# Optimization experiments

Hardware: AMD Instinct MI355X
Metric: run time of the kernel (lower is better)

The kernel has to match this reference:

```python
import jax, jax.numpy as jnp
import numpy as np

N = 50000          # nodes per node type
E = 1_600_000      # edges per canonical etype (avg degree 32)
IN_F = 385         # BERT_EMBEDDING_DIM(384) + NUMERICAL_FEATURES(1)
H = 128            # HIDDEN_DIM
# ntype order: 0=Policy, 1=Control, 2=ComplianceRequirement, 3=Risk
# etypes (src_ntype, dst_ntype): implements, mitigates, violates, addresses, informs
ETYPES = [(0, 1), (1, 3), (3, 2), (0, 2), (2, 0)]


def setup_inputs() -> dict:
    key = jax.random.key(0)
    ks = jax.random.split(key, 12)
    inp = {}
    names = ["feat_policy", "feat_control", "feat_compliance", "feat_risk"]
    for i, n in enumerate(names):
        inp[n] = jax.random.normal(ks[i], (N, IN_F), jnp.float32)
    inp["src"] = jax.random.randint(ks[4], (5, E), 0, N, jnp.int32)
    inp["dst"] = jax.random.randint(ks[5], (5, E), 0, N, jnp.int32)
    s_in = 1.0 / np.sqrt(IN_F).astype(np.float32)
    s_h = np.sqrt(6.0 / (H + H)).astype(np.float32)  # xavier_uniform for GraphConv
    inp["Wp"] = jax.random.uniform(ks[6], (4, IN_F, H), jnp.float32, -s_in, s_in)
    inp["bp"] = jax.random.uniform(ks[7], (4, H), jnp.float32, -s_in, s_in)
    inp["Wc1"] = jax.random.uniform(ks[8], (5, H, H), jnp.float32, -s_h, s_h)
    inp["bc1"] = jnp.zeros((5, H), jnp.float32)
    inp["Wc2"] = jax.random.uniform(ks[9], (5, H, H), jnp.float32, -s_h, s_h)
    inp["bc2"] = jnp.zeros((5, H), jnp.float32)
    return inp


def _graph_conv(x, s, d, W, b):
    """DGL GraphConv(norm='both'): D_dst^{-1/2} A D_src^{-1/2} X W + b."""
    ones = jnp.ones(s.shape[0], x.dtype)
    deg_out = jnp.clip(jax.ops.segment_sum(ones, s, num_segments=N), 1.0)
    deg_in = jnp.clip(jax.ops.segment_sum(ones, d, num_segments=N), 1.0)
    xs = x * jax.lax.rsqrt(deg_out)[:, None]            # [N, H] scale by src out-deg
    agg = jax.ops.segment_sum(xs[s], d, num_segments=N)  # gather + scatter-sum [N, H]
    agg = agg * jax.lax.rsqrt(deg_in)[:, None]
    return agg @ W + b


def reference(feat_policy, feat_control, feat_compliance, feat_risk,
              src, dst, Wp, bp, Wc1, bc1, Wc2, bc2):
    feats = [feat_policy, feat_control, feat_compliance, feat_risk]
    # input projections + relu per node type
    h = [jax.nn.relu(f @ Wp[i] + bp[i]) for i, f in enumerate(feats)]

    def hetero_layer(h, Wc, bc):
        out = [jnp.zeros((N, H), h[0].dtype) for _ in range(4)]
        for k, (st, dt) in enumerate(ETYPES):  # HeteroGraphConv aggregate='sum'
            out[dt] = out[dt] + _graph_conv(h[st], src[k], dst[k], Wc[k], bc[k])
        return out

    h = [jax.nn.relu(v) for v in hetero_layer(h, Wc1, bc1)]
    h = [jax.nn.relu(v) for v in hetero_layer(h, Wc2, bc2)]
    return jnp.stack(h)  # [4, N, H] final embeddings per node type
```

## Files before the change

### kernel.cpp

```cpp
#include <hip/hip_runtime.h>
#include <hip/hip_bf16.h>

#define INF 385
#define HD 128
#define NWG 16
#define HIST_BLOCKS (10 * NWG)

typedef __attribute__((ext_vector_type(8))) short short8;
typedef __attribute__((ext_vector_type(4))) float f32x4;

__device__ inline unsigned short f2b(float f) {
    __hip_bfloat16 h = __float2bfloat16(f);
    return *reinterpret_cast<unsigned short*>(&h);
}
__device__ inline float b2f(unsigned int lo16) {
    union { unsigned int u; float f; } c; c.u = lo16 << 16; return c.f;
}

__device__ __forceinline__ void convert_body(
    const float* f0, const float* f1, const float* f2, const float* f3,
    unsigned int* featB, float* alast, int N, int gid, int nthr)
{
    int per = N * 192;
    int tot = 4 * per;
    for (int p = gid; p < tot; p += nthr) {
        int t = p / per, rem = p - t * per;
        int n = rem / 192, c2 = (rem - n * 192) * 2;
        const float* f = (t < 2) ? (t == 0 ? f0 : f1) : (t == 2 ? f2 : f3);
        const float* row = f + (size_t)n * INF;
        float a = row[c2], b = row[c2 + 1];
        featB[p] = ((unsigned int)f2b(b) << 16) | f2b(a);
    }
    for (int p = gid; p < 4 * N; p += nthr) {
        int t = p / N, n = p - t * N;
        const float* f = (t < 2) ? (t == 0 ? f0 : f1) : (t == 2 ? f2 : f3);
        alast[p] = f[(size_t)n * INF + 384];
    }
}

__global__ __launch_bounds__(1024) void hist_conv_kernel(
    const int* __restrict__ src_all, const int* __restrict__ dst_all,
    unsigned short* __restrict__ partial,
    unsigned short* __restrict__ rank_local,
    int E, int N,
    const float* __restrict__ f0, const float* __restrict__ f1,
    const float* __restrict__ f2, const float* __restrict__ f3,
    unsigned int* __restrict__ featB, float* __restrict__ alast)
{
    __shared__ unsigned int cnt[25000];
    int tid = threadIdx.x;
    if (blockIdx.x >= HIST_BLOCKS) {
        int nconv = gridDim.x - HIST_BLOCKS;
        convert_body(f0, f1, f2, f3, featB, alast, N,
                     (blockIdx.x - HIST_BLOCKS) * 1024 + tid, nconv * 1024);
        return;
    }
    int g = blockIdx.x / NWG;
    int w = blockIdx.x % NWG;
    int half = (N + 1) / 2;
    for (int i = tid; i < half; i += 1024) cnt[i] = 0;
    __syncthreads();

    int C = (E + NWG - 1) / NWG;
    int lo = w * C, hi = min(lo + C, E);
    if (g < 5) {
        const int* arr = dst_all + (size_t)g * E;
        for (int e = lo + tid; e < hi; e += 1024) {
            int d = __builtin_nontemporal_load(&arr[e]);
            unsigned int sh = (d & 1) * 16;
            unsigned int old = atomicAdd(&cnt[d >> 1], 1u << sh);
            rank_local[(size_t)g * E + e] = (unsigned short)((old >> sh) & 0xffffu);
        }
    } else {
        const int* arr = src_all + (size_t)(g - 5) * E;
        for (int e = lo + tid; e < hi; e += 1024) {
            int d = __builtin_nontemporal_load(&arr[e]);
            atomicAdd(&cnt[d >> 1], 1u << ((d & 1) * 16));
        }
    }
    __syncthreads();
    unsigned short* outp = partial + ((size_t)g * NWG + w) * N;
    for (int n = tid; n < N; n += 1024)
        outp[n] = (unsigned short)((cnt[n >> 1] >> ((n & 1) * 16)) & 0xffffu);
}

__global__ void reduce_kernel(unsigned short* __restrict__ partial, int* __restrict__ cnt_dst,
                              float* __restrict__ rsq_out, float* __restrict__ rsq_in, int N) {
    int i = blockIdx.x * blockDim.x + threadIdx.x;
    int stride = gridDim.x * blockDim.x;
    int tot = 10 * N;
    for (; i < tot; i += stride) {
        int g = i / N, n = i - g * N;
        unsigned short* p = partial + ((size_t)g * NWG) * N + n;
        int sum = 0;
        #pragma unroll
        for (int w = 0; w < NWG; ++w) {
            int v = p[(size_t)w * N];
            p[(size_t)w * N] = (unsigned short)sum;
            sum += v;
        }
        float r = rsqrtf((float)max(sum, 1));
        if (g < 5) { cnt_dst[i] = sum; rsq_in[i] = r; }
        else rsq_out[i - 5 * N] = r;
    }
}

__global__ __launch_bounds__(1024) void scan_kernel(const int* __restrict__ cnt_all,
                                                    int* __restrict__ off_all, int n) {
    const int* cnt = cnt_all + (size_t)blockIdx.x * n;
    int* off = off_all + (size_t)blockIdx.x * (n + 1);
    __shared__ int ssum[1024];
    int t = threadIdx.x;
    int chunk = (n + 1023) / 1024;
    int lo = t * chunk, hi = min(lo + chunk, n);
    int s = 0;
    for (int i = lo; i < hi; ++i) s += cnt[i];
    ssum[t] = s;
    __syncthreads();
    for (int d = 1; d < 1024; d <<= 1) {
        int v = (t >= d) ? ssum[t - d] : 0;
        __syncthreads();
        ssum[t] += v;
        __syncthreads();
    }
    int excl = (t == 0) ? 0 : ssum[t - 1];
    for (int i = lo; i < hi; ++i) { off[i] = excl; excl += cnt[i]; }
    if (t == 1023) off[n] = ssum[1023];
}

__global__ __launch_bounds__(256) void permute_kernel(
    const int* __restrict__ src_all, const int* __restrict__ dst_all,
    const int* __restrict__ off, const unsigned short* __restrict__ partial,
    const unsigned short* __restrict__ rank_local,
    unsigned short* __restrict__ sorted, int E, int N)
{
    int gid = blockIdx.x * blockDim.x + threadIdx.x;
    int nthr = gridDim.x * blockDim.x;
    int tot = 5 * E;
    int C = (E + NWG - 1) / NWG;
    for (int i0 = gid * 4; i0 < tot; i0 += nthr * 4) {
        int d[4], s[4], rl[4];
        #pragma unroll
        for (int j = 0; j < 4; ++j) {
            d[j]  = __builtin_nontemporal_load(&dst_all[i0 + j]);
            s[j]  = __builtin_nontemporal_load(&src_all[i0 + j]);
            rl[j] = __builtin_nontemporal_load(&rank_local[i0 + j]);
        }
        int pos[4];
        #pragma unroll
        for (int j = 0; j < 4; ++j) {
            int i = i0 + j;
            int k = i / E, e = i - k * E;
            int w = e / C;
            pos[j] = off[(size_t)k * (N + 1) + d[j]]
                   + partial[((size_t)k * NWG + w) * N + d[j]]
                   + rl[j] + k * E;
        }
        #pragma unroll
        for (int j = 0; j < 4; ++j)
            __builtin_nontemporal_store((unsigned short)s[j], &sorted[pos[j]]);
    }
}

__global__ void convert_kernel(const float* __restrict__ f0, const float* __restrict__ f1,
                               const float* __restrict__ f2, const float* __restrict__ f3,
                               unsigned int* __restrict__ featB, float* __restrict__ alast, int N) {
    convert_body(f0, f1, f2, f3, featB, alast, N,
                 blockIdx.x * blockDim.x + threadIdx.x, gridDim.x * blockDim.x);
}

__global__ void prep_weights_kernel(const float* __restrict__ Wp,
                                    const float* __restrict__ Wc1, const float* __restrict__ Wc2,
                                    const float* __restrict__ bc1, const float* __restrict__ bc2,
                                    unsigned short* __restrict__ WpT,
                                    unsigned short* __restrict__ WcT,
                                    float* __restrict__ cbias) {
    int i = blockIdx.x * blockDim.x + threadIdx.x;
    int stride = gridDim.x * blockDim.x;
    const int nWp = 4 * 128 * 384;
    for (int p = i; p < nWp; p += stride) {
        int t = p / (128 * 384), rem = p % (128 * 384);
        int c = rem / 384, k = rem % 384;
        WpT[p] = f2b(Wp[(size_t)t * INF * HD + (size_t)k * HD + c]);
    }
    const int nWc = 5 * 128 * 128;
    for (int p = i; p < 2 * nWc; p += stride) {
        int layer = p / nWc, rem = p % nWc;
        int e = rem / (128 * 128), rem2 = rem % (128 * 128);
        int c = rem2 / 128, k = rem2 % 128;
        const float* W = layer ? Wc2 : Wc1;
        WcT[p] = f2b(W[(size_t)e * 128 * 128 + (size_t)k * 128 + c]);
    }
    for (int p = i; p < 2 * 4 * 128; p += stride) {
        int layer = p / 512, rem = p % 512;
        int t = rem / 128, c = rem % 128;
        const float* bc = layer ? bc2 : bc1;
        float v;
        if (t == 0) v = bc[4 * 128 + c];
        else if (t == 1) v = bc[0 * 128 + c];
        else if (t == 2) v = bc[2 * 128 + c] + bc[3 * 128 + c];
        else v = bc[1 * 128 + c];
        cbias[p] = v;
    }
}

struct GemmDesc {
    const unsigned short* A;
    const unsigned short* Bt;
    const float* bias;
    const float* rowscale;
    const float* alast;
    const float* wlast;
    unsigned short* out;
};
struct GemmBatch { GemmDesc d[5]; };

__global__ __launch_bounds__(256) void gemm_mfma_kernel(
    GemmBatch batch, int lda, int M, int K, int relu)
{
    const GemmDesc dsc = batch.d[blockIdx.y];
    const unsigned short* __restrict__ Bt = dsc.Bt;
    const unsigned short* __restrict__ A = dsc.A;

    __shared__ __align__(16) unsigned short As[64][72];
    __shared__ __align__(16) unsigned short Bs[128][72];
    const int tid = threadIdx.x;
    const int bm = blockIdx.x * 64;
    const int wid = tid >> 6, lane = tid & 63;
    const int wr = wid & 1, wc = wid >> 1;
    const int l15 = lane & 15, l4 = lane >> 4;

    f32x4 acc[2][4] = {};

    for (int k0 = 0; k0 < K; k0 += 64) {
        {
            int r = tid >> 2, q = tid & 3;
            int gm = bm + r;
            if (gm < M) {
                const uint4* g = (const uint4*)(A + (size_t)gm * lda + k0 + q * 16);
                *(uint4*)&As[r][q * 16] = g[0];
                *(uint4*)&As[r][q * 16 + 8] = g[1];
            } else {
                uint4 z = {0, 0, 0, 0};
                *(uint4*)&As[r][q * 16] = z;
                *(uint4*)&As[r][q * 16 + 8] = z;
            }
        }
        {
            int col = tid >> 1, hf = tid & 1;
            const uint4* g = (const uint4*)(Bt + (size_t)col * K + k0 + hf * 32);
            #pragma unroll
            for (int j = 0; j < 4; ++j)
                *(uint4*)&Bs[col][hf * 32 + j * 8] = g[j];
        }
        __syncthreads();
        #pragma unroll
        for (int kk = 0; kk < 2; ++kk) {
            short8 a[2], b[4];
            #pragma unroll
            for (int mi = 0; mi < 2; ++mi)
                a[mi] = *(const short8*)&As[wr * 32 + mi * 16 + l15][kk * 32 + l4 * 8];
            #pragma unroll
            for (int ni = 0; ni < 4; ++ni)
                b[ni] = *(const short8*)&Bs[wc * 64 + ni * 16 + l15][kk * 32 + l4 * 8];
            #pragma unroll
            for (int mi = 0; mi < 2; ++mi)
                #pragma unroll
                for (int ni = 0; ni < 4; ++ni)
                    acc[mi][ni] = __builtin_amdgcn_mfma_f32_16x16x32_bf16(
                        a[mi], b[ni], acc[mi][ni], 0, 0, 0);
        }
        __syncthreads();
    }

    #pragma unroll
    for (int mi = 0; mi < 2; ++mi) {
        #pragma unroll
        for (int r = 0; r < 4; ++r) {
            int grow = bm + wr * 32 + mi * 16 + l4 * 4 + r;
            if (grow >= M) continue;
            float rs = dsc.rowscale ? dsc.rowscale[grow] : 1.f;
            float al = dsc.alast ? dsc.alast[grow] : 0.f;
            #pragma unroll
            for (int ni = 0; ni < 4; ++ni) {
                int gcol = wc * 64 + ni * 16 + l15;
                float v = acc[mi][ni][r];
                if (dsc.wlast) v += al * dsc.wlast[gcol];
                if (dsc.bias) v += dsc.bias[gcol];
                v *= rs;
                if (relu) v = fmaxf(v, 0.f);
                dsc.out[(size_t)grow * HD + gcol] = f2b(v);
            }
        }
    }
}

struct GatherDesc {
    const unsigned short* msgA; const unsigned short* sortedA;
    const int* offA; const float* rsqA;
    const unsigned short* msgB; const unsigned short* sortedB;
    const int* offB; const float* rsqB;
    const float* bias; void* out;
};
struct GatherBatch { GatherDesc d[4]; };

__device__ __forceinline__ void accum8(uint4 v, float* acc) {
    acc[0] += b2f(v.x & 0xffffu); acc[1] += b2f(v.x >> 16);
    acc[2] += b2f(v.y & 0xffffu); acc[3] += b2f(v.y >> 16);
    acc[4] += b2f(v.z & 0xffffu); acc[5] += b2f(v.z >> 16);
    acc[6] += b2f(v.w & 0xffffu); acc[7] += b2f(v.w >> 16);
}

__device__ __forceinline__ void gather_seg(
    const unsigned short* __restrict__ msg, const unsigned short* __restrict__ sorted,
    int beg, int end, int sub, int lbyte, float* acc)
{
    const char* mbase = (const char*)msg;
    int e = beg;
    for (; e + 16 <= end; e += 16) {
        uint4 v[4];
        #pragma unroll
        for (int r = 0; r < 4; ++r) {
            int s = sorted[e + r * 4 + sub];
            v[r] = *(const uint4*)(mbase + (size_t)s * 256 + lbyte);
        }
        #pragma unroll
        for (int r = 0; r < 4; ++r) accum8(v[r], acc);
    }
    if (e < end) {
        #pragma unroll
        for (int r = 0; r < 4; ++r) {
            int idx = e + r * 4 + sub;
            if (idx < end) {
                int s = sorted[idx];
                uint4 v = *(const uint4*)(mbase + (size_t)s * 256 + lbyte);
                accum8(v, acc);
            }
        }
    }
}

template<int OUT_BF16>
__global__ __launch_bounds__(256) void gather_kernel(GatherBatch batch, int n)
{
    const GatherDesc d = batch.d[blockIdx.y];
    int node = blockIdx.x * 4 + (threadIdx.x >> 6);
    if (node >= n) return;
    int lane = threadIdx.x & 63;
    int sub = lane >> 4;
    int l16 = lane & 15;
    int lbyte = l16 * 16;

    float comb[8];
    {
        float acc[8] = {};
        gather_seg(d.msgA, d.sortedA, d.offA[node], d.offA[node + 1], sub, lbyte, acc);
        float rA = d.rsqA[node];
        if (d.msgB) {
            float acc2[8] = {};
            gather_seg(d.msgB, d.sortedB, d.offB[node], d.offB[node + 1], sub, lbyte, acc2);
            float rB = d.rsqB[node];
            #pragma unroll
            for (int c = 0; c < 8; ++c) comb[c] = acc[c] * rA + acc2[c] * rB;
        } else {
            #pragma unroll
            for (int c = 0; c < 8; ++c) comb[c] = acc[c] * rA;
        }
    }
    #pragma unroll
    for (int c = 0; c < 8; ++c) {
        comb[c] += __shfl_xor(comb[c], 16);
        comb[c] += __shfl_xor(comb[c], 32);
    }
    if (sub == 0) {
        const float* bptr = d.bias + l16 * 8;
        float4 b0 = *(const float4*)bptr;
        float4 b1 = *(const float4*)(bptr + 4);
        float o[8] = {comb[0] + b0.x, comb[1] + b0.y, comb[2] + b0.z, comb[3] + b0.w,
                      comb[4] + b1.x, comb[5] + b1.y, comb[6] + b1.z, comb[7] + b1.w};
        #pragma unroll
        for (int c = 0; c < 8; ++c) o[c] = fmaxf(o[c], 0.f);
        if (OUT_BF16) {
            uint4 pv;
            pv.x = ((unsigned int)f2b(o[1]) << 16) | f2b(o[0]);
            pv.y = ((unsigned int)f2b(o[3]) << 16) | f2b(o[2]);
            pv.z = ((unsigned int)f2b(o[5]) << 16) | f2b(o[4]);
            pv.w = ((unsigned int)f2b(o[7]) << 16) | f2b(o[6]);
            *(uint4*)((char*)d.out + (size_t)node * 256 + lbyte) = pv;
        } else {
            float4 f0 = {o[0], o[1], o[2], o[3]};
            float4 f1 = {o[4], o[5], o[6], o[7]};
            float4* op = (float4*)((char*)d.out + (size_t)node * 512 + (size_t)l16 * 32);
            op[0] = f0; op[1] = f1;
        }
    }
}

extern "C" void kernel_launch(void* const* d_in, const int* in_sizes, int n_in,
                              void* d_out, int out_size, void* d_ws, size_t ws_size,
                              hipStream_t stream)
{
    const float* feat[4] = {(const float*)d_in[0], (const float*)d_in[1],
                            (const float*)d_in[2], (const float*)d_in[3]};
    const int* src_all = (const int*)d_in[4];
    const int* dst_all = (const int*)d_in[5];
    const float* Wp  = (const float*)d_in[6];
    const float* bp  = (const float*)d_in[7];
    const float* Wc1 = (const float*)d_in[8];
    const float* bc1 = (const float*)d_in[9];
    const float* Wc2 = (const float*)d_in[10];
    const float* bc2 = (const float*)d_in[11];

    const int N = in_sizes[0] / INF;
    const int E = in_sizes[4] / 5;

    const int st_[5] = {0, 1, 3, 0, 2};

    char* w = (char*)d_ws;
    auto take = [&](size_t bytes) { char* p = w; w += (bytes + 255) & ~(size_t)255; return p; };
    int*   cnt_dst = (int*)take(5 * (size_t)N * 4);
    float* rsq_out = (float*)take(5 * (size_t)N * 4);
    float* rsq_in  = (float*)take(5 * (size_t)N * 4);
    int*   off     = (int*)take(5 * (size_t)(N + 1) * 4);
    unsigned short* sorted = (unsigned short*)take(5 * (size_t)E * 2);
    float* alast   = (float*)take(4 * (size_t)N * 4);
    unsigned short* WpT = (unsigned short*)take(4 * 128 * 384 * 2);
    unsigned short* WcT = (unsigned short*)take(2 * 5 * 128 * 128 * 2);
    float* cbias   = (float*)take(2 * 4 * 128 * 4);

    const size_t pr_bytes = 10u * NWG * (size_t)N * 2 + 5 * (size_t)E * 2;
    const size_t blob_sz = 4 * (size_t)N * 384 * 2;
    size_t fixed_used = (size_t)(w - (char*)d_ws);
    bool roomy = ws_size >= fixed_used + pr_bytes + blob_sz + (1u << 20);

    unsigned short *partial, *rank_local, *featB, *msg;
    if (roomy) {
        partial    = (unsigned short*)take(10u * NWG * (size_t)N * 2);
        rank_local = (unsigned short*)take(5 * (size_t)E * 2);
        char* blob = (char*)take(blob_sz);
        featB = (unsigned short*)blob;
        msg   = (unsigned short*)blob;
    } else {
        char* blob = (char*)take(blob_sz);
        partial    = (unsigned short*)blob;
        rank_local = (unsigned short*)(blob + 10u * NWG * (size_t)N * 2);
        featB      = (unsigned short*)blob;
        msg        = (unsigned short*)(blob + 32u * 1024 * 1024);
    }
    unsigned short* h0 = (unsigned short*)d_out;
    unsigned short* h1 = (unsigned short*)d_out + 4 * (size_t)N * HD;

    const int gblk = (N + 63) / 64;

    prep_weights_kernel<<<512, 256, 0, stream>>>(Wp, Wc1, Wc2, bc1, bc2, WpT, WcT, cbias);

    hist_conv_kernel<<<roomy ? HIST_BLOCKS + 512 : HIST_BLOCKS, 1024, 0, stream>>>(
        src_all, dst_all, partial, rank_local, E, N,
        feat[0], feat[1], feat[2], feat[3], (unsigned int*)featB, alast);
    reduce_kernel<<<(10 * N + 255) / 256, 256, 0, stream>>>(partial, cnt_dst, rsq_out, rsq_in, N);
    scan_kernel<<<5, 1024, 0, stream>>>(cnt_dst, off, N);
    permute_kernel<<<2048, 256, 0, stream>>>(src_all, dst_all, off, partial, rank_local,
                                             sorted, E, N);
    if (!roomy)
        convert_kernel<<<2048, 256, 0, stream>>>(feat[0], feat[1], feat[2], feat[3],
                                                 (unsigned int*)featB, alast, N);

    {
        GemmBatch pb = {};
        for (int t = 0; t < 4; ++t) {
            pb.d[t].A = featB + (size_t)t * N * 384;
            pb.d[t].Bt = WpT + (size_t)t * 128 * 384;
            pb.d[t].bias = bp + (size_t)t * HD;
            pb.d[t].rowscale = nullptr;
            pb.d[t].alast = alast + (size_t)t * N;
            pb.d[t].wlast = Wp + (size_t)t * INF * HD + 384 * HD;
            pb.d[t].out = h0 + (size_t)t * N * HD;
        }
        gemm_mfma_kernel<<<dim3(gblk, 4), 256, 0, stream>>>(pb, 384, N, 384, 1);
    }

    for (int layer = 0; layer < 2; ++layer) {
        const unsigned short* hin = layer ? h1 : h0;
        const unsigned short* WT = WcT + (size_t)layer * 5 * 128 * 128;
        const float* cb = cbias + (size_t)layer * 4 * 128;

        {
            GemmBatch cbch = {};
            for (int k = 0; k < 5; ++k) {
                cbch.d[k].A = hin + (size_t)st_[k] * N * HD;
                cbch.d[k].Bt = WT + (size_t)k * 128 * 128;
                cbch.d[k].bias = nullptr;
                cbch.d[k].rowscale = rsq_out + (size_t)k * N;
                cbch.d[k].alast = nullptr;
                cbch.d[k].wlast = nullptr;
                cbch.d[k].out = msg + (size_t)k * N * HD;
            }
            gemm_mfma_kernel<<<dim3(gblk, 5), 256, 0, stream>>>(cbch, HD, N, 128, 0);
        }

        {
            auto S = [&](int k) { return sorted + (size_t)k * E; };
            auto O = [&](int k) { return off + (size_t)k * (N + 1); };
            auto R = [&](int k) { return rsq_in + (size_t)k * N; };
            auto M_ = [&](int k) { return msg + (size_t)k * N * HD; };
            const int ksA[4] = {0, 1, 2, 4};
            const int dt [4] = {1, 3, 2, 0};
            GatherBatch gb = {};
            for (int y = 0; y < 4; ++y) {
                int k = ksA[y];
                gb.d[y].msgA = M_(k); gb.d[y].sortedA = S(k);
                gb.d[y].offA = O(k);  gb.d[y].rsqA = R(k);
                gb.d[y].msgB = nullptr; gb.d[y].sortedB = nullptr;
                gb.d[y].offB = nullptr; gb.d[y].rsqB = nullptr;
                gb.d[y].bias = cb + (size_t)dt[y] * HD;
                if (layer == 0)
                    gb.d[y].out = h1 + (size_t)dt[y] * N * HD;
                else
                    gb.d[y].out = (float*)d_out + (size_t)dt[y] * N * HD;
            }
            gb.d[2].msgB = M_(3); gb.d[2].sortedB = S(3);
            gb.d[2].offB = O(3);  gb.d[2].rsqB = R(3);
            const int gg = (N + 3) / 4;
            if (layer == 0)
                gather_kernel<1><<<dim3(gg, 4), 256, 0, stream>>>(gb, N);
            else
                gather_kernel<0><<<dim3(gg, 4), 256, 0, stream>>>(gb, N);
        }
    }
}
```

Before: 1.112 ms.

## Replace random-scatter permute with two-pass bucketed binning into staging buffers

Replaces the single permute pass, which scatters each edge's src id to a random position across the whole sorted array, with two passes. The first bins edges by destination-position range into 64 buckets per etype, using shared-memory counters and global cursors. The second scatters each bucket's entries within a 25K-element window so writes stay cache-local. This trades an extra 4-byte-per-edge staging write and read, a memset and two extra launches for better write locality. It only runs when the workspace is large enough.

```diff
diff --git a/kernel.cpp b/kernel.cpp
--- a/kernel.cpp
+++ b/kernel.cpp
@@ -5,6 +5,8 @@
 #define HD 128
 #define NWG 16
 #define HIST_BLOCKS (10 * NWG)
+#define NBUCKET 64
+#define BK_CHUNK 8192
 
 typedef __attribute__((ext_vector_type(8))) short short8;
 typedef __attribute__((ext_vector_type(4))) float f32x4;
@@ -128,6 +130,90 @@
     if (t == 1023) off[n] = ssum[1023];
 }
 
+__global__ __launch_bounds__(1024) void bin_kernel(
+    const int* __restrict__ src_all, const int* __restrict__ dst_all,
+    const int* __restrict__ off, const unsigned short* __restrict__ partial,
+    const unsigned short* __restrict__ rank_local,
+    int* __restrict__ cursor,
+    unsigned int* __restrict__ staging,
+    int E, int N, int W, int wgPerEt)
+{
+    __shared__ int pos_s[BK_CHUNK];
+    __shared__ unsigned short src_s[BK_CHUNK];
+    __shared__ int cntb[NBUCKET], gbase[NBUCKET], lcur[NBUCKET];
+    int k = blockIdx.x / wgPerEt;
+    int wg = blockIdx.x % wgPerEt;
+    int tid = threadIdx.x;
+    int lo = wg * BK_CHUNK, hi = min(lo + BK_CHUNK, E);
+    if (lo >= E) return;
+    if (tid < NBUCKET) cntb[tid] = 0;
+    __syncthreads();
+
+    int C = (E + NWG - 1) / NWG;
+    const int* srcs = src_all + (size_t)k * E;
+    const int* dsts = dst_all + (size_t)k * E;
+    const unsigned short* rl = rank_local + (size_t)k * E;
+    const int* offk = off + (size_t)k * (N + 1);
+    const unsigned short* pk = partial + (size_t)k * NWG * N;
+
+    #pragma unroll
+    for (int j = 0; j < BK_CHUNK / 1024; ++j) {
+        int idx = tid + j * 1024;
+        int e = lo + idx;
+        if (e < hi) {
+            int d = __builtin_nontemporal_load(&dsts[e]);
+            int s = __builtin_nontemporal_load(&srcs[e]);
+            int r = __builtin_nontemporal_load(&rl[e]);
+            int w = e / C;
+            int pos = offk[d] + pk[(size_t)w * N + d] + r;
+            pos_s[idx] = pos;
+            src_s[idx] = (unsigned short)s;
+            atomicAdd(&cntb[pos / W], 1);
+        }
+    }
+    __syncthreads();
+    if (tid < NBUCKET) {
+        gbase[tid] = atomicAdd(&cursor[k * NBUCKET + tid], cntb[tid]);
+        lcur[tid] = 0;
+    }
+    __syncthreads();
+    int cnt = hi - lo;
+    #pragma unroll
+    for (int j = 0; j < BK_CHUNK / 1024; ++j) {
+        int idx = tid + j * 1024;
+        if (idx < cnt) {
+            int pos = pos_s[idx];
+            int b = pos / W;
+            int l = atomicAdd(&lcur[b], 1);
+            unsigned int pair = ((unsigned int)src_s[idx] << 16) | (unsigned int)(pos - b * W);
+            staging[((size_t)k * NBUCKET + b) * W + gbase[b] + l] = pair;
+        }
+    }
+}
+
+__global__ __launch_bounds__(256) void unbucket_kernel(
+    const unsigned int* __restrict__ staging, const int* __restrict__ cursor,
+    unsigned short* __restrict__ sorted, int E, int W)
+{
+    int k = blockIdx.x / NBUCKET;
+    int b = blockIdx.x % NBUCKET;
+    int cnt = cursor[k * NBUCKET + b];
+    const unsigned int* stg = staging + ((size_t)k * NBUCKET + b) * W;
+    unsigned short* out = sorted + (size_t)k * E + (size_t)b * W;
+    int i = threadIdx.x;
+    for (; i + 768 < cnt; i += 1024) {
+        unsigned int p0 = stg[i], p1 = stg[i + 256], p2 = stg[i + 512], p3 = stg[i + 768];
+        out[p0 & 0xffffu] = (unsigned short)(p0 >> 16);
+        out[p1 & 0xffffu] = (unsigned short)(p1 >> 16);
+        out[p2 & 0xffffu] = (unsigned short)(p2 >> 16);
+        out[p3 & 0xffffu] = (unsigned short)(p3 >> 16);
+    }
+    for (; i < cnt; i += 256) {
+        unsigned int p0 = stg[i];
+        out[p0 & 0xffffu] = (unsigned short)(p0 >> 16);
+    }
+}
+
 __global__ __launch_bounds__(256) void permute_kernel(
     const int* __restrict__ src_all, const int* __restrict__ dst_all,
     const int* __restrict__ off, const unsigned short* __restrict__ partial,
@@ -146,19 +232,16 @@
             s[j]  = __builtin_nontemporal_load(&src_all[i0 + j]);
             rl[j] = __builtin_nontemporal_load(&rank_local[i0 + j]);
         }
-        int pos[4];
         #pragma unroll
         for (int j = 0; j < 4; ++j) {
             int i = i0 + j;
             int k = i / E, e = i - k * E;
             int w = e / C;
-            pos[j] = off[(size_t)k * (N + 1) + d[j]]
-                   + partial[((size_t)k * NWG + w) * N + d[j]]
-                   + rl[j] + k * E;
-        }
-        #pragma unroll
-        for (int j = 0; j < 4; ++j)
-            __builtin_nontemporal_store((unsigned short)s[j], &sorted[pos[j]]);
+            int pos = off[(size_t)k * (N + 1) + d[j]]
+                    + partial[((size_t)k * NWG + w) * N + d[j]]
+                    + rl[j] + k * E;
+            __builtin_nontemporal_store((unsigned short)s[j], &sorted[pos]);
+        }
     }
 }
 
@@ -413,6 +496,7 @@
 
     const int N = in_sizes[0] / INF;
     const int E = in_sizes[4] / 5;
+    const int W = (E + NBUCKET - 1) / NBUCKET;
 
     const int st_[5] = {0, 1, 3, 0, 2};
 
@@ -427,16 +511,21 @@
     unsigned short* WpT = (unsigned short*)take(4 * 128 * 384 * 2);
     unsigned short* WcT = (unsigned short*)take(2 * 5 * 128 * 128 * 2);
     float* cbias   = (float*)take(2 * 4 * 128 * 4);
-
-    const size_t pr_bytes = 10u * NWG * (size_t)N * 2 + 5 * (size_t)E * 2;
-    const size_t blob_sz = 4 * (size_t)N * 384 * 2;
+    int*   cursor  = (int*)take(5 * NBUCKET * 4);
+
+    const size_t pr_bytes  = 10u * NWG * (size_t)N * 2 + 5 * (size_t)E * 2;
+    const size_t stg_bytes = 5 * (size_t)NBUCKET * (size_t)W * 4;
+    const size_t blob_sz   = 4 * (size_t)N * 384 * 2;
     size_t fixed_used = (size_t)(w - (char*)d_ws);
-    bool roomy = ws_size >= fixed_used + pr_bytes + blob_sz + (1u << 20);
+    bool roomy  = ws_size >= fixed_used + pr_bytes + blob_sz + (1u << 20);
+    bool staged = ws_size >= fixed_used + pr_bytes + stg_bytes + blob_sz + (1u << 20);
 
     unsigned short *partial, *rank_local, *featB, *msg;
+    unsigned int* staging = nullptr;
     if (roomy) {
         partial    = (unsigned short*)take(10u * NWG * (size_t)N * 2);
         rank_local = (unsigned short*)take(5 * (size_t)E * 2);
+        if (staged) staging = (unsigned int*)take(stg_bytes);
         char* blob = (char*)take(blob_sz);
         featB = (unsigned short*)blob;
         msg   = (unsigned short*)blob;
@@ -459,8 +548,17 @@
         feat[0], feat[1], feat[2], feat[3], (unsigned int*)featB, alast);
     reduce_kernel<<<(10 * N + 255) / 256, 256, 0, stream>>>(partial, cnt_dst, rsq_out, rsq_in, N);
     scan_kernel<<<5, 1024, 0, stream>>>(cnt_dst, off, N);
-    permute_kernel<<<2048, 256, 0, stream>>>(src_all, dst_all, off, partial, rank_local,
-                                             sorted, E, N);
+
+    if (staged) {
+        hipMemsetAsync(cursor, 0, 5 * NBUCKET * 4, stream);
+        int wgPerEt = (E + BK_CHUNK - 1) / BK_CHUNK;
+        bin_kernel<<<5 * wgPerEt, 1024, 0, stream>>>(
+            src_all, dst_all, off, partial, rank_local, cursor, staging, E, N, W, wgPerEt);
+        unbucket_kernel<<<5 * NBUCKET, 256, 0, stream>>>(staging, cursor, sorted, E, W);
+    } else {
+        permute_kernel<<<2048, 256, 0, stream>>>(src_all, dst_all, off, partial, rank_local,
+                                                 sorted, E, N);
+    }
     if (!roomy)
         convert_kernel<<<2048, 256, 0, stream>>>(feat[0], feat[1], feat[2], feat[3],
                                                  (unsigned int*)featB, alast, N);
```

New measurement: 1.017 ms. -8.6%, faster.
